# Kernel tuning notes

Hardware: AMD Instinct MI355X
Metric: run time of the kernel (lower is better)

The kernel has to match this reference:

```python
import jax, jax.numpy as jnp
import numpy as np

B, S, D, H, M = 2, 2048, 1024, 16, 40
DH = D // H  # 64
L = S + M    # kv length after memory concat


def setup_inputs() -> dict:
    key = jax.random.key(0)
    ks = jax.random.split(key, 20)
    s = 1.0 / np.sqrt(D)
    inp = {
        'v': jax.random.normal(ks[0], (B, S, D), jnp.float32),
        'k': jax.random.normal(ks[1], (B, S, D), jnp.float32),
        'q': jax.random.normal(ks[2], (B, S, D), jnp.float32),
        # additive binary mask (1 = masked out), broadcast over heads
        'mask': jax.random.randint(ks[3], (B, 1, S, L), 0, 2).astype(jnp.float32),
        'Wq': jax.random.normal(ks[4], (D, D), jnp.float32) * s,
        'bq': jnp.zeros((D,), jnp.float32),
        'Wk': jax.random.normal(ks[5], (D, D), jnp.float32) * s,
        'bk': jnp.zeros((D,), jnp.float32),
        'Wv': jax.random.normal(ks[6], (D, D), jnp.float32) * s,
        'bv': jnp.zeros((D,), jnp.float32),
        'k_memory': jax.random.normal(ks[7], (1, M, D), jnp.float32) * (1.0 / np.sqrt(DH)),
        'v_memory': jax.random.normal(ks[8], (1, M, D), jnp.float32) * (1.0 / np.sqrt(M)),
        'Wkm': jax.random.normal(ks[9], (D, D), jnp.float32) * s,
        'bkm': jnp.zeros((D,), jnp.float32),
        'Wvm': jax.random.normal(ks[10], (D, D), jnp.float32) * s,
        'bvm': jnp.zeros((D,), jnp.float32),
        'Wo': jax.random.normal(ks[11], (D, D), jnp.float32) * s,
        'bo': jnp.zeros((D,), jnp.float32),
    }
    return inp


def _split_heads(x):
    # [B, T, D] -> [B, H, T, DH]
    b, t, _ = x.shape
    return x.reshape(b, t, H, DH).transpose(0, 2, 1, 3)


def reference(v, k, q, mask, Wq, bq, Wk, bk, Wv, bv, k_memory, v_memory,
              Wkm, bkm, Wvm, bvm, Wo, bo):
    qp = q @ Wq + bq
    kp = k @ Wk + bk
    vp = v @ Wv + bv
    km = (k_memory @ Wkm + bkm)  # [1, M, D]
    vm = (v_memory @ Wvm + bvm)  # [1, M, D]
    kc = jnp.concatenate([kp, jnp.broadcast_to(km, (kp.shape[0], M, D))], axis=1)
    vc = jnp.concatenate([vp, jnp.broadcast_to(vm, (vp.shape[0], M, D))], axis=1)
    qh, kh, vh = _split_heads(qp), _split_heads(kc), _split_heads(vc)
    # scores: [B, H, S, L]
    scores = jnp.einsum('bhqd,bhkd->bhqk', qh, kh) / np.sqrt(DH)
    scores = scores + mask * (-1e9)
    attn = jax.nn.softmax(scores, axis=-1)
    ctx = jnp.einsum('bhqk,bhkd->bhqd', attn, vh)  # [B, H, S, DH]
    ctx = ctx.transpose(0, 2, 1, 3).reshape(ctx.shape[0], S, D)
    out = ctx @ Wo + bo
    return (out, attn)
```

## Files before the change

kernel.cpp:

```cpp
#include <hip/hip_runtime.h>
#include <hip/hip_bf16.h>

typedef __attribute__((ext_vector_type(8))) short short8v;
typedef __attribute__((ext_vector_type(4))) short short4v;
typedef __attribute__((ext_vector_type(4))) float f32x4;

constexpr int B_ = 2, S_ = 2048, H_ = 16, MM_ = 40;
constexpr int L_ = S_ + MM_;
constexpr int LP_ = 2112;
constexpr int NT_ = 33;
constexpr float QSCALE = 0.18033688011112042f;

struct S2 { short hi, lo; };
__device__ __forceinline__ S2 split2(float f) {
    unsigned u = __builtin_bit_cast(unsigned, f);
    short hi = (short)(u >> 16);
    float fh = __builtin_bit_cast(float, u & 0xFFFF0000u);
    float fl = f - fh;
    short lo = (short)(__builtin_bit_cast(unsigned, fl) >> 16);
    return {hi, lo};
}
__device__ __forceinline__ short f2bh(float f) {
    unsigned u = __builtin_bit_cast(unsigned, f);
    u = (u + 0x7FFFu + ((u >> 16) & 1u)) >> 16;
    return (short)u;
}
__device__ __forceinline__ f32x4 mfma16(short8v a, short8v b, f32x4 c) {
    return __builtin_amdgcn_mfma_f32_16x16x32_bf16(a, b, c, 0, 0, 0);
}
__device__ __forceinline__ unsigned cvt_pk_bf16(float a, float b) {
    unsigned r;
    asm("v_cvt_pk_bf16_f32 %0, %1, %2" : "=v"(r) : "v"(a), "v"(b));
    return r;
}

__global__ __launch_bounds__(64) void mask_pack(
    const float* __restrict__ mask, unsigned* __restrict__ mp)
{
    const int row = blockIdx.x;
    const float* mr = mask + (size_t)row * L_;
    unsigned* orow = mp + (size_t)row * 68;
    for (int wd = threadIdx.x; wd < 66; wd += 64) {
        int l0 = wd * 32;
        unsigned bits = 0u;
        int lim = (wd < 65) ? 32 : 8;
        for (int j = 0; j < lim; j += 4) {
            float4 m4 = *(const float4*)(mr + l0 + j);
            bits |= ((unsigned)(m4.x != 0.f)) << (j + 0);
            bits |= ((unsigned)(m4.y != 0.f)) << (j + 1);
            bits |= ((unsigned)(m4.z != 0.f)) << (j + 2);
            bits |= ((unsigned)(m4.w != 0.f)) << (j + 3);
        }
        if (wd == 65) bits |= 0xFFFFFF00u;
        orow[wd] = bits;
    }
}

__global__ __launch_bounds__(256) void wsplit6_kernel(
    const float* __restrict__ W0, const float* __restrict__ W1,
    const float* __restrict__ W2, const float* __restrict__ W3,
    const float* __restrict__ W4, const float* __restrict__ W5,
    short* __restrict__ WT)
{
    const float* Ws[6] = {W0, W1, W2, W3, W4, W5};
    const float* W = Ws[blockIdx.z];
    short* WTh = WT + (size_t)blockIdx.z * 2097152;
    short* WTl = WTh + 1048576;
    __shared__ float T[64][68];
    const int t = threadIdx.x;
    const int k0 = blockIdx.x * 64, n0 = blockIdx.y * 64;
    {
        int r = t >> 2, c = (t & 3) * 16;
        const float* src = W + (size_t)(k0 + r) * 1024 + n0 + c;
        *(float4*)&T[r][c + 0]  = *(const float4*)(src + 0);
        *(float4*)&T[r][c + 4]  = *(const float4*)(src + 4);
        *(float4*)&T[r][c + 8]  = *(const float4*)(src + 8);
        *(float4*)&T[r][c + 12] = *(const float4*)(src + 12);
    }
    __syncthreads();
    {
        int n = t >> 2, ks = (t & 3) * 16;
        short8v h0, h1, l0, l1;
#pragma unroll
        for (int j = 0; j < 8; ++j) {
            S2 a = split2(T[ks + j][n]);     h0[j] = a.hi; l0[j] = a.lo;
            S2 b = split2(T[ks + 8 + j][n]); h1[j] = b.hi; l1[j] = b.lo;
        }
        size_t dst = (size_t)(n0 + n) * 1024 + k0 + ks;
        *(short8v*)(WTh + dst) = h0;  *(short8v*)(WTh + dst + 8) = h1;
        *(short8v*)(WTl + dst) = l0;  *(short8v*)(WTl + dst + 8) = l1;
    }
}

__global__ __launch_bounds__(256) void pad_clear(short* __restrict__ Vh)
{
    int idx = blockIdx.x * 256 + threadIdx.x;
    if (idx >= 2048 * 24) return;
    int rd = idx / 24, l = L_ + idx % 24;
    Vh[(size_t)rd * LP_ + l] = 0;
}

template<int ASRC>
__device__ __forceinline__ void gemm_core(
    const float* __restrict__ Af, const short* __restrict__ Ahg,
    const short* __restrict__ Alg, const short* __restrict__ WTh,
    const short* __restrict__ WTl, const float* __restrict__ bias, float scale,
    short* __restrict__ Oh, short* __restrict__ Ol, float* __restrict__ Of,
    int M, int RPB, int TD, int loff, int omode, int bx, int by)
{
    __shared__ short Ah[128][40];
    __shared__ short Al[128][40];
    __shared__ short Bh[128][40];
    __shared__ short Bl[128][40];
    const int tid = threadIdx.x;
    const int lane = tid & 63, wid = tid >> 6;
    const int wr = wid >> 1, wc = wid & 1;
    const int row0 = by * 128, col0 = bx * 128;
    const int sr = tid >> 1, sc = (tid & 1) << 4;

    f32x4 acc[4][4] = {};

    for (int k0 = 0; k0 < 1024; k0 += 32) {
        if (ASRC == 0) {
            float f[16];
            int gr = row0 + sr;
            if (gr < M) {
                const float* ap = Af + (size_t)gr * 1024 + k0 + sc;
                float4 a0 = *(const float4*)(ap + 0);
                float4 a1 = *(const float4*)(ap + 4);
                float4 a2 = *(const float4*)(ap + 8);
                float4 a3 = *(const float4*)(ap + 12);
                f[0]=a0.x; f[1]=a0.y; f[2]=a0.z; f[3]=a0.w;
                f[4]=a1.x; f[5]=a1.y; f[6]=a1.z; f[7]=a1.w;
                f[8]=a2.x; f[9]=a2.y; f[10]=a2.z; f[11]=a2.w;
                f[12]=a3.x; f[13]=a3.y; f[14]=a3.z; f[15]=a3.w;
            } else {
#pragma unroll
                for (int j = 0; j < 16; ++j) f[j] = 0.f;
            }
            short8v h0, h1, l0, l1;
#pragma unroll
            for (int j = 0; j < 8; ++j) {
                S2 s = split2(f[j]); h0[j] = s.hi; l0[j] = s.lo;
            }
#pragma unroll
            for (int j = 0; j < 8; ++j) {
                S2 s = split2(f[8 + j]); h1[j] = s.hi; l1[j] = s.lo;
            }
            *(short8v*)&Ah[sr][sc] = h0; *(short8v*)&Ah[sr][sc + 8] = h1;
            *(short8v*)&Al[sr][sc] = l0; *(short8v*)&Al[sr][sc + 8] = l1;
        } else {
            const short* ah = Ahg + (size_t)(row0 + sr) * 1024 + k0 + sc;
            const short* al = Alg + (size_t)(row0 + sr) * 1024 + k0 + sc;
            *(short8v*)&Ah[sr][sc]     = *(const short8v*)ah;
            *(short8v*)&Ah[sr][sc + 8] = *(const short8v*)(ah + 8);
            *(short8v*)&Al[sr][sc]     = *(const short8v*)al;
            *(short8v*)&Al[sr][sc + 8] = *(const short8v*)(al + 8);
        }
        {
            const short* bh = WTh + (size_t)(col0 + sr) * 1024 + k0 + sc;
            const short* bl = WTl + (size_t)(col0 + sr) * 1024 + k0 + sc;
            *(short8v*)&Bh[sr][sc]     = *(const short8v*)bh;
            *(short8v*)&Bh[sr][sc + 8] = *(const short8v*)(bh + 8);
            *(short8v*)&Bl[sr][sc]     = *(const short8v*)bl;
            *(short8v*)&Bl[sr][sc + 8] = *(const short8v*)(bl + 8);
        }
        __syncthreads();
        const int kof = (lane >> 4) << 3;
        const int ar = lane & 15;
        short8v afh[4], afl[4], bfh[4], bfl[4];
#pragma unroll
        for (int i = 0; i < 4; ++i) {
            afh[i] = *(const short8v*)&Ah[wr * 64 + i * 16 + ar][kof];
            afl[i] = *(const short8v*)&Al[wr * 64 + i * 16 + ar][kof];
            bfh[i] = *(const short8v*)&Bh[wc * 64 + i * 16 + ar][kof];
            bfl[i] = *(const short8v*)&Bl[wc * 64 + i * 16 + ar][kof];
        }
#pragma unroll
        for (int i = 0; i < 4; ++i)
#pragma unroll
            for (int j = 0; j < 4; ++j) {
                acc[i][j] = mfma16(afh[i], bfh[j], acc[i][j]);
                acc[i][j] = mfma16(afh[i], bfl[j], acc[i][j]);
                acc[i][j] = mfma16(afl[i], bfh[j], acc[i][j]);
            }
        __syncthreads();
    }

#pragma unroll
    for (int i = 0; i < 4; ++i) {
#pragma unroll
        for (int j = 0; j < 4; ++j) {
            int colb = col0 + wc * 64 + j * 16 + (lane & 15);
            float bv = bias[colb];
            int rowb = row0 + wr * 64 + i * 16 + ((lane >> 4) << 2);
            if (omode == 2) {
                if (rowb < M) {
                    int bb = rowb / RPB, tt = rowb % RPB;
                    int hh = colb >> 6, dh = colb & 63;
                    short4v hs;
#pragma unroll
                    for (int r = 0; r < 4; ++r)
                        hs[r] = f2bh((acc[i][j][r] + bv) * scale);
                    size_t dst = ((size_t)(bb * H_ + hh) * 64 + dh) * LP_ + loff + tt;
                    *(short4v*)(Oh + dst) = hs;
                }
            } else {
#pragma unroll
                for (int r = 0; r < 4; ++r) {
                    int row = rowb + r;
                    if (row < M) {
                        float o = (acc[i][j][r] + bv) * scale;
                        int bb = row / RPB, tt = row % RPB;
                        if (omode == 0) {
                            Of[((size_t)bb * TD + loff + tt) * 1024 + colb] = o;
                        } else {
                            int hh = colb >> 6, dh = colb & 63;
                            size_t dst = ((size_t)(bb * H_ + hh) * TD + loff + tt) * 64 + dh;
                            S2 s = split2(o);
                            Oh[dst] = s.hi; Ol[dst] = s.lo;
                        }
                    }
                }
            }
        }
    }
}

__global__ __launch_bounds__(256) void qkv_gemm(
    const float* __restrict__ q_in, const float* __restrict__ k_in,
    const float* __restrict__ v_in, const short* __restrict__ WT,
    const float* __restrict__ bq, const float* __restrict__ bk,
    const float* __restrict__ bv,
    short* __restrict__ Qh, short* __restrict__ Ql,
    short* __restrict__ Kh, short* __restrict__ Kl, short* __restrict__ Vh)
{
    const int z = blockIdx.z;
    const float* A = (z == 0) ? q_in : (z == 1) ? k_in : v_in;
    const short* WTh = WT + (size_t)z * 2097152;
    const short* WTl = WTh + 1048576;
    const float* bias = (z == 0) ? bq : (z == 1) ? bk : bv;
    float scale = (z == 0) ? QSCALE : 1.0f;
    short* Oh = (z == 0) ? Qh : (z == 1) ? Kh : Vh;
    short* Ol = (z == 0) ? Ql : Kl;
    int omode = (z == 2) ? 2 : 1;
    int TD = (z == 0) ? S_ : LP_;
    gemm_core<0>(A, nullptr, nullptr, WTh, WTl, bias, scale,
                 Oh, Ol, nullptr, 4096, 2048, TD, 0, omode,
                 blockIdx.x, blockIdx.y);
}

__global__ __launch_bounds__(256) void mem_gemm(
    const float* __restrict__ kmem, const float* __restrict__ vmem,
    const short* __restrict__ WT,
    const float* __restrict__ bkm, const float* __restrict__ bvm,
    short* __restrict__ Kh, short* __restrict__ Kl, short* __restrict__ Vh)
{
    const int z = blockIdx.z;
    const int which = z >> 1, b = z & 1;
    const float* A = which ? vmem : kmem;
    const short* WTh = WT + (size_t)(3 + which) * 2097152;
    const short* WTl = WTh + 1048576;
    const float* bias = which ? bvm : bkm;
    short* Oh = which ? (Vh + (size_t)b * H_ * 64 * LP_)
                      : (Kh + (size_t)b * H_ * LP_ * 64);
    short* Ol = which ? nullptr : (Kl + (size_t)b * H_ * LP_ * 64);
    gemm_core<0>(A, nullptr, nullptr, WTh, WTl, bias, 1.0f,
                 Oh, Ol, nullptr, 40, 40, LP_, S_, which ? 2 : 1,
                 blockIdx.x, blockIdx.y);
}

__global__ __launch_bounds__(256) void out_gemm(
    const short* __restrict__ Ch, const short* __restrict__ Cl,
    const short* __restrict__ WT, const float* __restrict__ bo,
    float* __restrict__ outp)
{
    const short* WTh = WT + (size_t)5 * 2097152;
    gemm_core<1>(nullptr, Ch, Cl, WTh, WTh + 1048576, bo, 1.0f,
                 nullptr, nullptr, outp, 4096, 2048, S_, 0, 0,
                 blockIdx.x, blockIdx.y);
}

__global__ __launch_bounds__(128) void attn4_kernel(
    const short* __restrict__ Qh, const short* __restrict__ Ql,
    const short* __restrict__ Kh, const short* __restrict__ Kl,
    const short* __restrict__ Vh, const unsigned* __restrict__ mp,
    float* __restrict__ attn, float* __restrict__ invg,
    short* __restrict__ Ch, short* __restrict__ Cl)
{
    __shared__ short KhB[2][64][64];
    __shared__ short KlB[2][64][64];
    __shared__ short VB[2][64][64];
    __shared__ short Ph[2][16][68];
    __shared__ float sbuf[2][16];

    const int id = blockIdx.x;
    const int wg = (id & 7) * 256 + (id >> 3);
    const int bh = wg >> 6, qb = wg & 63;
    const int b = bh >> 4, h = bh & 15;
    const int lane = threadIdx.x & 63, w = threadIdx.x >> 6;
    const int lq = lane & 15, hi = lane >> 4;
    const int sw = lq & 7;
    const int q0 = qb * 32 + w * 16;
    const int q = q0 + lq;

    const char* kh_g = (const char*)(Kh + (size_t)bh * LP_ * 64);
    const char* kl_g = (const char*)(Kl + (size_t)bh * LP_ * 64);
    const char* v_g  = (const char*)(Vh + (size_t)bh * 64 * LP_);

    auto stage_k = [&](int buf, int tt) {
#pragma unroll
        for (int i = 0; i < 4; ++i) {
            int o = w * 4096 + i * 1024 + lane * 16;
            int r = o >> 7, c = (o >> 4) & 7;
            int cs = c ^ (r & 7);
            const char* sh = kh_g + (size_t)tt * 8192 + r * 128 + cs * 16;
            const char* sl = kl_g + (size_t)tt * 8192 + r * 128 + cs * 16;
            __builtin_amdgcn_global_load_lds((const void*)sh,
                (void*)((char*)&KhB[buf][0][0] + w * 4096 + i * 1024), 16, 0, 0);
            __builtin_amdgcn_global_load_lds((const void*)sl,
                (void*)((char*)&KlB[buf][0][0] + w * 4096 + i * 1024), 16, 0, 0);
        }
    };
    auto stage_v = [&](int buf, int tt) {
#pragma unroll
        for (int i = 0; i < 4; ++i) {
            int o = w * 4096 + i * 1024 + lane * 16;
            int dh = o >> 7, c = (o >> 4) & 7;
            int cs = c ^ (dh & 7);
            const char* src = v_g + (size_t)dh * (LP_ * 2) + (size_t)tt * 128 + cs * 16;
            __builtin_amdgcn_global_load_lds((const void*)src,
                (void*)((char*)&VB[buf][0][0] + w * 4096 + i * 1024), 16, 0, 0);
        }
    };

    const size_t qbase = ((size_t)bh * S_ + q) * 64 + hi * 8;
    const short8v qh0 = *(const short8v*)(Qh + qbase);
    const short8v qh1 = *(const short8v*)(Qh + qbase + 32);
    const short8v ql0 = *(const short8v*)(Ql + qbase);
    const short8v ql1 = *(const short8v*)(Ql + qbase + 32);
    const unsigned* mrow = mp + ((size_t)b * S_ + q) * 68;
    short* arow = (short*)(attn + ((size_t)bh * S_ + q) * L_);

    float sm = 0.f;
    f32x4 pv[4] = {};

    stage_k(0, 0);
    stage_v(0, 0);
    __syncthreads();

    int cur = 0;
    for (int t = 0; t < NT_; ++t) {
        if (t < NT_ - 1) { stage_k(cur ^ 1, t + 1); stage_v(cur ^ 1, t + 1); }

        const unsigned w0 = mrow[2 * t], w1 = mrow[2 * t + 1];
        const short8v* kp = (const short8v*)&KhB[cur][0][0];
        const short8v* lp = (const short8v*)&KlB[cur][0][0];
#pragma unroll
        for (int ls = 0; ls < 4; ++ls) {
            const int r = ls * 16 + lq;
            const short8v kh0 = kp[r * 8 + (hi ^ sw)];
            const short8v kh1 = kp[r * 8 + ((hi + 4) ^ sw)];
            const short8v kl0 = lp[r * 8 + (hi ^ sw)];
            const short8v kl1 = lp[r * 8 + ((hi + 4) ^ sw)];
            __builtin_amdgcn_s_setprio(1);
            f32x4 acc = {0.f, 0.f, 0.f, 0.f};
            acc = mfma16(kh0, qh0, acc); acc = mfma16(kh1, qh1, acc);
            acc = mfma16(kh0, ql0, acc); acc = mfma16(kh1, ql1, acc);
            acc = mfma16(kl0, qh0, acc); acc = mfma16(kl1, qh1, acc);
            __builtin_amdgcn_s_setprio(0);
            const unsigned wb = (ls & 2) ? w1 : w0;
            const int sh = (ls & 1) * 16 + hi * 4;
            float pr[4];
#pragma unroll
            for (int r2 = 0; r2 < 4; ++r2) {
                float e = __builtin_exp2f(acc[r2]);
                pr[r2] = ((wb >> (sh + r2)) & 1u) ? 0.f : e;
            }
            sm += (pr[0] + pr[1]) + (pr[2] + pr[3]);
            unsigned pk0 = cvt_pk_bf16(pr[0], pr[1]);
            unsigned pk1 = cvt_pk_bf16(pr[2], pr[3]);
            const int lbase = t * 64 + ls * 16 + hi * 4;
            if (t < NT_ - 1 || lbase + 3 < L_)
                *(uint2*)(arow + lbase) = uint2{pk0, pk1};
            *(uint2*)&Ph[w][lq][ls * 16 + hi * 4] = uint2{pk0, pk1};
        }
        {
            const short8v pa0 = *(const short8v*)&Ph[w][lq][hi * 8];
            const short8v pa1 = *(const short8v*)&Ph[w][lq][32 + hi * 8];
            const short8v* vp = (const short8v*)&VB[cur][0][0];
            __builtin_amdgcn_s_setprio(1);
#pragma unroll
            for (int j = 0; j < 4; ++j)
                pv[j] = mfma16(pa0, vp[(j * 16 + lq) * 8 + (hi ^ sw)], pv[j]);
#pragma unroll
            for (int j = 0; j < 4; ++j)
                pv[j] = mfma16(pa1, vp[(j * 16 + lq) * 8 + ((hi + 4) ^ sw)], pv[j]);
            __builtin_amdgcn_s_setprio(0);
        }
        __syncthreads();
        cur ^= 1;
    }

    sm += __shfl_xor(sm, 16);
    sm += __shfl_xor(sm, 32);
    if (lane < 16) sbuf[w][lane] = sm;
    __syncthreads();
    if (lane < 16) {
        float sv = sbuf[w][lane];
        invg[(size_t)bh * S_ + q0 + lane] = sv > 0.f ? 1.0f / sv : 0.f;
    }
    float iv[4];
#pragma unroll
    for (int r = 0; r < 4; ++r) {
        float sv = sbuf[w][hi * 4 + r];
        iv[r] = sv > 0.f ? 1.0f / sv : 0.f;
    }
#pragma unroll
    for (int j = 0; j < 4; ++j)
#pragma unroll
        for (int r = 0; r < 4; ++r) {
            float o = pv[j][r] * iv[r];
            size_t dst = ((size_t)b * S_ + q0 + hi * 4 + r) * 1024 + h * 64 + j * 16 + lq;
            S2 sp = split2(o);
            Ch[dst] = sp.hi; Cl[dst] = sp.lo;
        }
}

__global__ __launch_bounds__(256) void norm_attn(
    float* __restrict__ attn, const float* __restrict__ invg)
{
    __shared__ unsigned rowbuf[1044];
    const int row = blockIdx.x;
    const float iv = invg[row];
    float* rowp = attn + (size_t)row * L_;
    const unsigned* src = (const unsigned*)rowp;
    for (int i = threadIdx.x; i < 1044; i += 256) rowbuf[i] = src[i];
    __syncthreads();
    float4* dst = (float4*)rowp;
    for (int j = threadIdx.x; j < 522; j += 256) {
        unsigned u0 = rowbuf[2 * j], u1 = rowbuf[2 * j + 1];
        float4 v;
        v.x = __builtin_bit_cast(float, u0 << 16) * iv;
        v.y = __builtin_bit_cast(float, u0 & 0xFFFF0000u) * iv;
        v.z = __builtin_bit_cast(float, u1 << 16) * iv;
        v.w = __builtin_bit_cast(float, u1 & 0xFFFF0000u) * iv;
        dst[j] = v;
    }
}

extern "C" void kernel_launch(void* const* d_in, const int* in_sizes, int n_in,
                              void* d_out, int out_size, void* d_ws, size_t ws_size,
                              hipStream_t stream)
{
    const float* v_in = (const float*)d_in[0];
    const float* k_in = (const float*)d_in[1];
    const float* q_in = (const float*)d_in[2];
    const float* mask = (const float*)d_in[3];
    const float* Wq = (const float*)d_in[4];  const float* bq = (const float*)d_in[5];
    const float* Wk = (const float*)d_in[6];  const float* bk = (const float*)d_in[7];
    const float* Wv = (const float*)d_in[8];  const float* bv = (const float*)d_in[9];
    const float* kmem = (const float*)d_in[10];
    const float* vmem = (const float*)d_in[11];
    const float* Wkm = (const float*)d_in[12]; const float* bkm = (const float*)d_in[13];
    const float* Wvm = (const float*)d_in[14]; const float* bvm = (const float*)d_in[15];
    const float* Wo = (const float*)d_in[16];  const float* bo = (const float*)d_in[17];

    char* wsb = (char*)d_ws;
    short* WT  = (short*)(wsb);
    short* Qhb = (short*)(wsb + 25165824);
    short* Qlb = (short*)(wsb + 33554432);
    short* Khb = (short*)(wsb + 41943040);
    short* Klb = (short*)(wsb + 50593792);
    short* Vhb = (short*)(wsb + 59244544);
    short* Chb = (short*)(wsb + 67895296);
    short* Clb = (short*)(wsb + 76283904);
    float* invb = (float*)(wsb + 84672512);
    unsigned* mp = (unsigned*)(wsb + 84934656);
    if (ws_size < 86048768) return;

    float* outp = (float*)d_out;
    float* attnp = outp + (size_t)B_ * S_ * 1024;

    dim3 blk(256);

    mask_pack<<<dim3(B_ * S_), dim3(64), 0, stream>>>(mask, mp);
    wsplit6_kernel<<<dim3(16, 16, 6), blk, 0, stream>>>(Wq, Wk, Wv, Wkm, Wvm, Wo, WT);

    qkv_gemm<<<dim3(8, 32, 3), blk, 0, stream>>>(
        q_in, k_in, v_in, WT, bq, bk, bv, Qhb, Qlb, Khb, Klb, Vhb);

    mem_gemm<<<dim3(8, 1, 4), blk, 0, stream>>>(
        kmem, vmem, WT, bkm, bvm, Khb, Klb, Vhb);
    pad_clear<<<dim3(192), blk, 0, stream>>>(Vhb);

    attn4_kernel<<<dim3(2048), dim3(128), 0, stream>>>(
        Qhb, Qlb, Khb, Klb, Vhb, mp, attnp, invb, Chb, Clb);
    norm_attn<<<dim3(B_ * H_ * S_), blk, 0, stream>>>(attnp, invb);

    out_gemm<<<dim3(8, 32), blk, 0, stream>>>(Chb, Clb, WT, bo, outp);
}
```

Before: 683.8 us.

## Merge mask packing into QKV GEMM, fuse output GEMM with attn normalization, coalesce attn stores

Mask bit-packing now runs as an extra z-slice of the QKV GEMM launch, and the output projection GEMM shares one launch with a grid-strided attention-row normalization, so independent work overlaps and launch count drops. Inside the attention kernel, bf16 probability stores go through the LDS P tile and are written as 16-byte row-contiguous chunks instead of scattered 8-byte stores. The risks are load imbalance between the heterogeneous block types and the extra LDS reads in the attention loop.

```diff
diff --git a/kernel.cpp b/kernel.cpp
--- a/kernel.cpp
+++ b/kernel.cpp
@@ -32,28 +32,6 @@
     unsigned r;
     asm("v_cvt_pk_bf16_f32 %0, %1, %2" : "=v"(r) : "v"(a), "v"(b));
     return r;
-}
-
-__global__ __launch_bounds__(64) void mask_pack(
-    const float* __restrict__ mask, unsigned* __restrict__ mp)
-{
-    const int row = blockIdx.x;
-    const float* mr = mask + (size_t)row * L_;
-    unsigned* orow = mp + (size_t)row * 68;
-    for (int wd = threadIdx.x; wd < 66; wd += 64) {
-        int l0 = wd * 32;
-        unsigned bits = 0u;
-        int lim = (wd < 65) ? 32 : 8;
-        for (int j = 0; j < lim; j += 4) {
-            float4 m4 = *(const float4*)(mr + l0 + j);
-            bits |= ((unsigned)(m4.x != 0.f)) << (j + 0);
-            bits |= ((unsigned)(m4.y != 0.f)) << (j + 1);
-            bits |= ((unsigned)(m4.z != 0.f)) << (j + 2);
-            bits |= ((unsigned)(m4.w != 0.f)) << (j + 3);
-        }
-        if (wd == 65) bits |= 0xFFFFFF00u;
-        orow[wd] = bits;
-    }
 }
 
 __global__ __launch_bounds__(256) void wsplit6_kernel(
@@ -233,9 +211,33 @@
     const float* __restrict__ bq, const float* __restrict__ bk,
     const float* __restrict__ bv,
     short* __restrict__ Qh, short* __restrict__ Ql,
-    short* __restrict__ Kh, short* __restrict__ Kl, short* __restrict__ Vh)
+    short* __restrict__ Kh, short* __restrict__ Kl, short* __restrict__ Vh,
+    const float* __restrict__ mask, unsigned* __restrict__ mp)
 {
     const int z = blockIdx.z;
+    if (z == 3) {
+        const int blk = blockIdx.y * 8 + blockIdx.x;
+        for (int rr = 0; rr < 16; ++rr) {
+            const int row = blk * 16 + rr;
+            const float* mr = mask + (size_t)row * L_;
+            unsigned* orow = mp + (size_t)row * 68;
+            for (int wd = threadIdx.x; wd < 66; wd += 256) {
+                int l0 = wd * 32;
+                unsigned bits = 0u;
+                int lim = (wd < 65) ? 32 : 8;
+                for (int j = 0; j < lim; j += 4) {
+                    float4 m4 = *(const float4*)(mr + l0 + j);
+                    bits |= ((unsigned)(m4.x != 0.f)) << (j + 0);
+                    bits |= ((unsigned)(m4.y != 0.f)) << (j + 1);
+                    bits |= ((unsigned)(m4.z != 0.f)) << (j + 2);
+                    bits |= ((unsigned)(m4.w != 0.f)) << (j + 3);
+                }
+                if (wd == 65) bits |= 0xFFFFFF00u;
+                orow[wd] = bits;
+            }
+        }
+        return;
+    }
     const float* A = (z == 0) ? q_in : (z == 1) ? k_in : v_in;
     const short* WTh = WT + (size_t)z * 2097152;
     const short* WTl = WTh + 1048576;
@@ -270,17 +272,6 @@
                  blockIdx.x, blockIdx.y);
 }
 
-__global__ __launch_bounds__(256) void out_gemm(
-    const short* __restrict__ Ch, const short* __restrict__ Cl,
-    const short* __restrict__ WT, const float* __restrict__ bo,
-    float* __restrict__ outp)
-{
-    const short* WTh = WT + (size_t)5 * 2097152;
-    gemm_core<1>(nullptr, Ch, Cl, WTh, WTh + 1048576, bo, 1.0f,
-                 nullptr, nullptr, outp, 4096, 2048, S_, 0, 0,
-                 blockIdx.x, blockIdx.y);
-}
-
 __global__ __launch_bounds__(128) void attn4_kernel(
     const short* __restrict__ Qh, const short* __restrict__ Ql,
     const short* __restrict__ Kh, const short* __restrict__ Kl,
@@ -340,7 +331,9 @@
     const short8v ql0 = *(const short8v*)(Ql + qbase);
     const short8v ql1 = *(const short8v*)(Ql + qbase + 32);
     const unsigned* mrow = mp + ((size_t)b * S_ + q) * 68;
-    short* arow = (short*)(attn + ((size_t)bh * S_ + q) * L_);
+
+    const int dr = lane >> 2, dc = lane & 3;
+    short* dbase = (short*)(attn + ((size_t)bh * S_ + q0 + dr) * L_);
 
     float sm = 0.f;
     f32x4 pv[4] = {};
@@ -380,10 +373,19 @@
             sm += (pr[0] + pr[1]) + (pr[2] + pr[3]);
             unsigned pk0 = cvt_pk_bf16(pr[0], pr[1]);
             unsigned pk1 = cvt_pk_bf16(pr[2], pr[3]);
-            const int lbase = t * 64 + ls * 16 + hi * 4;
-            if (t < NT_ - 1 || lbase + 3 < L_)
-                *(uint2*)(arow + lbase) = uint2{pk0, pk1};
             *(uint2*)&Ph[w][lq][ls * 16 + hi * 4] = uint2{pk0, pk1};
+        }
+        {
+            short8v v0 = *(const short8v*)&Ph[w][dr][dc * 8];
+            short8v v1 = *(const short8v*)&Ph[w][dr][32 + dc * 8];
+            short* dst = dbase + t * 64 + dc * 8;
+            if (t < NT_ - 1) {
+                *(short8v*)dst = v0;
+                *(short8v*)(dst + 32) = v1;
+            } else {
+                *(short8v*)dst = v0;
+                if (dc == 0) *(short8v*)(dst + 32) = v1;
+            }
         }
         {
             const short8v pa0 = *(const short8v*)&Ph[w][lq][hi * 8];
@@ -427,25 +429,38 @@
         }
 }
 
-__global__ __launch_bounds__(256) void norm_attn(
-    float* __restrict__ attn, const float* __restrict__ invg)
-{
+__global__ __launch_bounds__(256) void tail_kernel(
+    const short* __restrict__ Ch, const short* __restrict__ Cl,
+    const short* __restrict__ WT, const float* __restrict__ bo,
+    float* __restrict__ outp, float* __restrict__ attn,
+    const float* __restrict__ invg)
+{
+    if (blockIdx.x < 256) {
+        const short* WTh = WT + (size_t)5 * 2097152;
+        gemm_core<1>(nullptr, Ch, Cl, WTh, WTh + 1048576, bo, 1.0f,
+                     nullptr, nullptr, outp, 4096, 2048, S_, 0, 0,
+                     blockIdx.x & 7, blockIdx.x >> 3);
+        return;
+    }
     __shared__ unsigned rowbuf[1044];
-    const int row = blockIdx.x;
-    const float iv = invg[row];
-    float* rowp = attn + (size_t)row * L_;
-    const unsigned* src = (const unsigned*)rowp;
-    for (int i = threadIdx.x; i < 1044; i += 256) rowbuf[i] = src[i];
-    __syncthreads();
-    float4* dst = (float4*)rowp;
-    for (int j = threadIdx.x; j < 522; j += 256) {
-        unsigned u0 = rowbuf[2 * j], u1 = rowbuf[2 * j + 1];
-        float4 v;
-        v.x = __builtin_bit_cast(float, u0 << 16) * iv;
-        v.y = __builtin_bit_cast(float, u0 & 0xFFFF0000u) * iv;
-        v.z = __builtin_bit_cast(float, u1 << 16) * iv;
-        v.w = __builtin_bit_cast(float, u1 & 0xFFFF0000u) * iv;
-        dst[j] = v;
+    const int nb = blockIdx.x - 256;
+    for (int row = nb; row < B_ * H_ * S_; row += 2048) {
+        const float iv = invg[row];
+        float* rowp = attn + (size_t)row * L_;
+        const unsigned* src = (const unsigned*)rowp;
+        __syncthreads();
+        for (int i = threadIdx.x; i < 1044; i += 256) rowbuf[i] = src[i];
+        __syncthreads();
+        float4* dst = (float4*)rowp;
+        for (int j = threadIdx.x; j < 522; j += 256) {
+            unsigned u0 = rowbuf[2 * j], u1 = rowbuf[2 * j + 1];
+            float4 v;
+            v.x = __builtin_bit_cast(float, u0 << 16) * iv;
+            v.y = __builtin_bit_cast(float, u0 & 0xFFFF0000u) * iv;
+            v.z = __builtin_bit_cast(float, u1 << 16) * iv;
+            v.w = __builtin_bit_cast(float, u1 & 0xFFFF0000u) * iv;
+            dst[j] = v;
+        }
     }
 }
 
@@ -484,11 +499,10 @@
 
     dim3 blk(256);
 
-    mask_pack<<<dim3(B_ * S_), dim3(64), 0, stream>>>(mask, mp);
     wsplit6_kernel<<<dim3(16, 16, 6), blk, 0, stream>>>(Wq, Wk, Wv, Wkm, Wvm, Wo, WT);
 
-    qkv_gemm<<<dim3(8, 32, 3), blk, 0, stream>>>(
-        q_in, k_in, v_in, WT, bq, bk, bv, Qhb, Qlb, Khb, Klb, Vhb);
+    qkv_gemm<<<dim3(8, 32, 4), blk, 0, stream>>>(
+        q_in, k_in, v_in, WT, bq, bk, bv, Qhb, Qlb, Khb, Klb, Vhb, mask, mp);
 
     mem_gemm<<<dim3(8, 1, 4), blk, 0, stream>>>(
         kmem, vmem, WT, bkm, bvm, Khb, Klb, Vhb);
@@ -496,7 +510,7 @@
 
     attn4_kernel<<<dim3(2048), dim3(128), 0, stream>>>(
         Qhb, Qlb, Khb, Klb, Vhb, mp, attnp, invb, Chb, Clb);
-    norm_attn<<<dim3(B_ * H_ * S_), blk, 0, stream>>>(attnp, invb);
-
-    out_gemm<<<dim3(8, 32), blk, 0, stream>>>(Chb, Clb, WT, bo, outp);
-}
+
+    tail_kernel<<<dim3(2304), blk, 0, stream>>>(
+        Chb, Clb, WT, bo, outp, attnp, invb);
+}
```

Measured after the change: 894.2 us. 30.8% more time.
